# Performance work log

Hardware: AMD Instinct MI355X
Metric: run time of the kernel (lower is better)

The kernel has to match this reference:

```python
import jax, jax.numpy as jnp
import numpy as np

RANK = 16
ALPHA = 32.0
LORA_SCALE = ALPHA / RANK  # 2.0


def setup_inputs() -> dict:
    key = jax.random.key(0)
    ks = jax.random.split(key, 7)
    B_, S, D_IN, D_OUT = 4, 2048, 4096, 4096
    x = jax.random.normal(ks[0], (B_, S, D_IN), dtype=jnp.float32)
    qweight = jax.random.randint(ks[1], (D_OUT, D_IN), 0, 16, dtype=jnp.int32)
    w_min = jax.random.normal(ks[2], (D_OUT, 1), dtype=jnp.float32) * 0.1
    # row scale ~ (max-min)/15 of typical weights; keep positive
    w_scale = jax.random.uniform(ks[3], (D_OUT, 1), dtype=jnp.float32, minval=1e-3, maxval=0.02)
    bias = jax.random.normal(ks[4], (D_OUT,), dtype=jnp.float32) * 0.02
    A = jax.random.normal(ks[5], (RANK, D_IN), dtype=jnp.float32) * 0.02
    # module inits B to zeros; use small randn so the LoRA branch is exercised
    Bm = jax.random.normal(ks[6], (D_OUT, RANK), dtype=jnp.float32) * 0.02
    return {"x": x, "qweight": qweight, "w_min": w_min, "w_scale": w_scale,
            "bias": bias, "A": A, "B": Bm}


def reference(x, qweight, w_min, w_scale, bias, A, B):
    # Row-wise 4-bit dequant: W[o,i] = q[o,i]*scale[o] + min[o]
    base_weight = qweight.astype(jnp.float32) * w_scale + w_min  # [O, I]
    base_out = jnp.einsum('bsi,oi->bso', x, base_weight) + bias   # [B, S, O]
    # LoRA: (x @ A^T) @ B^T * (alpha/rank); dropout p=0 is identity
    lora_out = jnp.einsum('bsr,or->bso', jnp.einsum('bsi,ri->bsr', x, A), B) * LORA_SCALE
    return base_out + lora_out
```

## Files before the change

### kernel.cpp

```cpp
#include <hip/hip_runtime.h>
#include <hip/hip_bf16.h>

typedef unsigned short u16;
typedef unsigned int u32;
typedef __bf16 bf16x8 __attribute__((ext_vector_type(8)));
typedef float f32x4 __attribute__((ext_vector_type(4)));
typedef int i32x4 __attribute__((ext_vector_type(4)));
typedef u16 u16x4 __attribute__((ext_vector_type(4)));
typedef u16 u16x8 __attribute__((ext_vector_type(8)));

#define D_IN 4096
#define D_OUT 4096
#define M_TOT 8192
#define RANK_ 16

#define BM 256
#define BN 256
#define BK 64
#define NT (D_IN / BK)
#define OPB 2
#define DQ_BLOCKS (D_OUT / OPB)
#define XC_BLOCKS ((M_TOT * D_IN) / (256 * 8))

__device__ __forceinline__ u16 f2bf(float f) {
    union { float f; u32 u; } v; v.f = f;
    u32 u = v.u;
    u32 r = (u + 0x7FFFu + ((u >> 16) & 1u)) >> 16;
    return (u16)r;
}

__global__ __launch_bounds__(256) void producer_kernel(
        const int* __restrict__ q, const float* __restrict__ wmin,
        const float* __restrict__ wscale, const float* __restrict__ A,
        const float* __restrict__ Bm, const float* __restrict__ x,
        u16* __restrict__ Wb, u16* __restrict__ Xb) {
    const int K = D_IN;
    if (blockIdx.x < DQ_BLOCKS) {
        int o0 = blockIdx.x * OPB;
        float s0 = wscale[o0], s1 = wscale[o0 + 1];
        float m0 = wmin[o0],   m1 = wmin[o0 + 1];
        float Br0[RANK_], Br1[RANK_];
        #pragma unroll
        for (int r = 0; r < RANK_; ++r) {
            Br0[r] = 2.0f * Bm[(size_t)o0 * RANK_ + r];
            Br1[r] = 2.0f * Bm[(size_t)(o0 + 1) * RANK_ + r];
        }
        for (int i4 = threadIdx.x; i4 < K / 4; i4 += 256) {
            int i = i4 * 4;
            i32x4 q0 = __builtin_nontemporal_load((const i32x4*)(q + (size_t)o0 * K + i));
            i32x4 q1 = __builtin_nontemporal_load((const i32x4*)(q + (size_t)(o0 + 1) * K + i));
            float v00 = (float)q0.x * s0 + m0, v01 = (float)q0.y * s0 + m0;
            float v02 = (float)q0.z * s0 + m0, v03 = (float)q0.w * s0 + m0;
            float v10 = (float)q1.x * s1 + m1, v11 = (float)q1.y * s1 + m1;
            float v12 = (float)q1.z * s1 + m1, v13 = (float)q1.w * s1 + m1;
            #pragma unroll
            for (int r = 0; r < RANK_; ++r) {
                f32x4 av = *(const f32x4*)(A + (size_t)r * K + i);
                v00 += Br0[r] * av.x; v01 += Br0[r] * av.y;
                v02 += Br0[r] * av.z; v03 += Br0[r] * av.w;
                v10 += Br1[r] * av.x; v11 += Br1[r] * av.y;
                v12 += Br1[r] * av.z; v13 += Br1[r] * av.w;
            }
            u16x4 o0v, o1v;
            o0v.x = f2bf(v00); o0v.y = f2bf(v01); o0v.z = f2bf(v02); o0v.w = f2bf(v03);
            o1v.x = f2bf(v10); o1v.y = f2bf(v11); o1v.z = f2bf(v12); o1v.w = f2bf(v13);
            *(u16x4*)(Wb + (size_t)o0 * K + i) = o0v;
            *(u16x4*)(Wb + (size_t)(o0 + 1) * K + i) = o1v;
        }
    } else {
        size_t i = (size_t)(blockIdx.x - DQ_BLOCKS) * 256 + threadIdx.x;
        const f32x4* p = (const f32x4*)x + i * 2;
        f32x4 a = __builtin_nontemporal_load(p);
        f32x4 b = __builtin_nontemporal_load(p + 1);
        u16x8 o;
        o[0] = f2bf(a.x); o[1] = f2bf(a.y); o[2] = f2bf(a.z); o[3] = f2bf(a.w);
        o[4] = f2bf(b.x); o[5] = f2bf(b.y); o[6] = f2bf(b.z); o[7] = f2bf(b.w);
        *(u16x8*)(Xb + i * 8) = o;
    }
}


#define STAGE_R(sarr, larr, base, kt) do { _Pragma("unroll") \
    for (int j_ = 0; j_ < 2; ++j_) \
        __builtin_amdgcn_global_load_lds( \
            (__attribute__((address_space(1))) u32*)(sarr[j_] + (kt) * 64), \
            (__attribute__((address_space(3))) u32*)(smem + (base) + larr[j_]), \
            16, 0, 0); } while (0)

#define MFMA(d, va, vb) d = __builtin_amdgcn_mfma_f32_16x16x32_bf16(va, vb, d, 0, 0, 0)

__global__ __launch_bounds__(512, 2) void gemm_bt_kernel(const u16* __restrict__ Xb,
                                                         const u16* __restrict__ Wb,
                                                         const float* __restrict__ bias,
                                                         float* __restrict__ out) {
    extern __shared__ __align__(16) char smem[];
    const int K = D_IN, N = D_OUT;

    int bid = blockIdx.x;
    int swz = (bid & 7) * 64 + (bid >> 3);
    int tM = swz >> 4;
    int tN = swz & 15;

    int t = threadIdx.x;
    int lane = t & 63;
    int wave = t >> 6;
    int wm = wave >> 2;
    int wn = wave & 3;
    int lr = lane & 15;
    int hi = lane >> 4;
    int l7 = lane & 7;

    int xs0 = ((0 * 4 + hi) ^ l7) << 4;
    int xs1 = ((1 * 4 + hi) ^ l7) << 4;
    int aRow = (wm * 128 + lr) * 128;
    int bRow = (wn * 64 + lr) * 128;

    const u16 *srcA03[2], *srcA47[2], *srcB01[2], *srcB23[2];
    int ldsA03[2], ldsA47[2], ldsB01[2], ldsB23[2];
    #pragma unroll
    for (int j = 0; j < 2; ++j) {
        int idx = j * 512 + t;
        int rl = idx >> 3, slot = idx & 7;
        int rA = (rl & 63) + ((rl >> 6) << 7);
        int rB = (rl & 31) + ((rl >> 5) << 6);
        int r = rA;
        ldsA03[j] = r * 128 + slot * 16;
        srcA03[j] = Xb + (size_t)(tM * 256 + r) * K + ((slot ^ (r & 7)) << 3);
        r = rA + 64;
        ldsA47[j] = r * 128 + slot * 16;
        srcA47[j] = Xb + (size_t)(tM * 256 + r) * K + ((slot ^ (r & 7)) << 3);
        r = rB;
        ldsB01[j] = r * 128 + slot * 16;
        srcB01[j] = Wb + (size_t)(tN * 256 + r) * K + ((slot ^ (r & 7)) << 3);
        r = rB + 32;
        ldsB23[j] = r * 128 + slot * 16;
        srcB23[j] = Wb + (size_t)(tN * 256 + r) * K + ((slot ^ (r & 7)) << 3);
    }

    f32x4 acc[8][4];
    #pragma unroll
    for (int i = 0; i < 8; ++i)
        #pragma unroll
        for (int j = 0; j < 4; ++j)
            acc[i][j] = (f32x4){0.f, 0.f, 0.f, 0.f};

    STAGE_R(srcA03, ldsA03, 0, 0);     STAGE_R(srcA47, ldsA47, 0, 0);
    STAGE_R(srcB01, ldsB01, 65536, 0); STAGE_R(srcB23, ldsB23, 65536, 0);
    STAGE_R(srcA03, ldsA03, 32768, 1); STAGE_R(srcA47, ldsA47, 32768, 1);
    STAGE_R(srcB01, ldsB01, 98304, 1); STAGE_R(srcB23, ldsB23, 98304, 1);
    asm volatile("s_waitcnt vmcnt(8)" ::: "memory");
    __builtin_amdgcn_s_barrier();

    bf16x8 a[4][2], b23[2][2], b01[2][2];
    #pragma unroll
    for (int nf = 0; nf < 2; ++nf) {
        b01[nf][0] = *(const bf16x8*)(smem + 65536 + bRow + nf * 2048 + xs0);
        b01[nf][1] = *(const bf16x8*)(smem + 65536 + bRow + nf * 2048 + xs1);
    }
    #pragma unroll
    for (int mf = 0; mf < 4; ++mf) {
        a[mf][0] = *(const bf16x8*)(smem + aRow + mf * 2048 + xs0);
        a[mf][1] = *(const bf16x8*)(smem + aRow + mf * 2048 + xs1);
    }
    #pragma unroll
    for (int nf = 0; nf < 2; ++nf) {
        b23[nf][0] = *(const bf16x8*)(smem + 65536 + bRow + (nf + 2) * 2048 + xs0);
        b23[nf][1] = *(const bf16x8*)(smem + 65536 + bRow + (nf + 2) * 2048 + xs1);
    }

    for (int tt = 0; tt < NT; ++tt) {
        int pA = (tt & 1) * 32768;
        int pB = 65536 + (tt & 1) * 32768;
        int pBn = 65536 + ((~tt) & 1) * 32768;
        int pAn = ((~tt) & 1) * 32768;
        bool pre = (tt + 2 < NT);

        if (pre) { STAGE_R(srcB01, ldsB01, pB, tt + 2); }
        __builtin_amdgcn_s_barrier();
        asm volatile("s_waitcnt lgkmcnt(4)");
        __builtin_amdgcn_s_setprio(1);
        #pragma unroll
        for (int mf = 0; mf < 4; ++mf)
            #pragma unroll
            for (int nf = 0; nf < 2; ++nf) {
                MFMA(acc[mf][nf], a[mf][0], b01[nf][0]);
                MFMA(acc[mf][nf], a[mf][1], b01[nf][1]);
            }
        __builtin_amdgcn_s_setprio(0);
        __builtin_amdgcn_s_barrier();

        if (pre) { STAGE_R(srcA03, ldsA03, pA, tt + 2); }
        __builtin_amdgcn_s_barrier();
        asm volatile("s_waitcnt lgkmcnt(0)");
        __builtin_amdgcn_s_setprio(1);
        #pragma unroll
        for (int mf = 0; mf < 4; ++mf)
            #pragma unroll
            for (int nf = 0; nf < 2; ++nf) {
                MFMA(acc[mf][nf + 2], a[mf][0], b23[nf][0]);
                MFMA(acc[mf][nf + 2], a[mf][1], b23[nf][1]);
            }
        __builtin_amdgcn_s_setprio(0);
        #pragma unroll
        for (int mf = 0; mf < 4; ++mf) {
            a[mf][0] = *(const bf16x8*)(smem + pA + aRow + (mf + 4) * 2048 + xs0);
            a[mf][1] = *(const bf16x8*)(smem + pA + aRow + (mf + 4) * 2048 + xs1);
        }
        __builtin_amdgcn_s_barrier();

        if (pre) { STAGE_R(srcB23, ldsB23, pB, tt + 2); }
        __builtin_amdgcn_s_barrier();
        asm volatile("s_waitcnt lgkmcnt(0)");
        __builtin_amdgcn_s_setprio(1);
        #pragma unroll
        for (int mf = 0; mf < 4; ++mf)
            #pragma unroll
            for (int nf = 0; nf < 2; ++nf) {
                MFMA(acc[mf + 4][nf], a[mf][0], b01[nf][0]);
                MFMA(acc[mf + 4][nf], a[mf][1], b01[nf][1]);
            }
        __builtin_amdgcn_s_setprio(0);
        __builtin_amdgcn_s_barrier();

        if (pre) { STAGE_R(srcA47, ldsA47, pA, tt + 2); }
        if (tt < NT - 2) { asm volatile("s_waitcnt vmcnt(8)" ::: "memory"); }
        else             { asm volatile("s_waitcnt vmcnt(0)" ::: "memory"); }
        __builtin_amdgcn_s_barrier();
        if (tt + 1 < NT) {
            #pragma unroll
            for (int nf = 0; nf < 2; ++nf) {
                b01[nf][0] = *(const bf16x8*)(smem + pBn + bRow + nf * 2048 + xs0);
                b01[nf][1] = *(const bf16x8*)(smem + pBn + bRow + nf * 2048 + xs1);
            }
        }
        __builtin_amdgcn_s_setprio(1);
        #pragma unroll
        for (int mf = 0; mf < 4; ++mf)
            #pragma unroll
            for (int nf = 0; nf < 2; ++nf) {
                MFMA(acc[mf + 4][nf + 2], a[mf][0], b23[nf][0]);
                MFMA(acc[mf + 4][nf + 2], a[mf][1], b23[nf][1]);
            }
        __builtin_amdgcn_s_setprio(0);
        if (tt + 1 < NT) {
            #pragma unroll
            for (int mf = 0; mf < 4; ++mf) {
                a[mf][0] = *(const bf16x8*)(smem + pAn + aRow + mf * 2048 + xs0);
                a[mf][1] = *(const bf16x8*)(smem + pAn + aRow + mf * 2048 + xs1);
            }
            #pragma unroll
            for (int nf = 0; nf < 2; ++nf) {
                b23[nf][0] = *(const bf16x8*)(smem + pBn + bRow + (nf + 2) * 2048 + xs0);
                b23[nf][1] = *(const bf16x8*)(smem + pBn + bRow + (nf + 2) * 2048 + xs1);
            }
        }
        __builtin_amdgcn_s_barrier();
    }

    #pragma unroll
    for (int nf = 0; nf < 4; ++nf) {
        int gn = tN * 256 + wn * 64 + nf * 16 + lr;
        float bs = bias[gn];
        #pragma unroll
        for (int mf = 0; mf < 8; ++mf) {
            #pragma unroll
            for (int r = 0; r < 4; ++r) {
                int gm = tM * 256 + wm * 128 + mf * 16 + hi * 4 + r;
                out[(size_t)gm * N + gn] = acc[mf][nf][r] + bs;
            }
        }
    }
}

extern "C" void kernel_launch(void* const* d_in, const int* in_sizes, int n_in,
                              void* d_out, int out_size, void* d_ws, size_t ws_size,
                              hipStream_t stream) {
    (void)in_sizes; (void)n_in; (void)out_size; (void)ws_size;
    const float* x      = (const float*)d_in[0];
    const int*   qw     = (const int*)d_in[1];
    const float* wmin   = (const float*)d_in[2];
    const float* wscale = (const float*)d_in[3];
    const float* bias   = (const float*)d_in[4];
    const float* A      = (const float*)d_in[5];
    const float* Bm     = (const float*)d_in[6];
    float* out = (float*)d_out;

    u16* Wb = (u16*)d_ws;
    u16* Xb = Wb + (size_t)D_OUT * D_IN;

    producer_kernel<<<DQ_BLOCKS + XC_BLOCKS, 256, 0, stream>>>(
        qw, wmin, wscale, A, Bm, x, Wb, Xb);
    gemm_bt_kernel<<<(M_TOT / BM) * (D_OUT / BN), 512, 131072, stream>>>(Xb, Wb, bias, out);
}
```

Measured before the change: 276.9 us.

## Make GEMM blocks compute two N tiles each and overlap the epilogue with prefetch

The grid is halved to 256 blocks, and each block computes two output tiles in sequence: column tiles tN0 and tN0+8 for the same M row. The first K-tiles of the second tile are prefetched into LDS while the first tile's epilogue stores are written. This aims to hide the store epilogue and the pipeline warm-up behind loads and to match the grid to the CU count (256 blocks at 2 blocks per CU). The risk is a longer serial chain per block and less load balancing across CUs.

```diff
diff --git a/kernel.cpp b/kernel.cpp
--- a/kernel.cpp
+++ b/kernel.cpp
@@ -21,6 +21,7 @@
 #define OPB 2
 #define DQ_BLOCKS (D_OUT / OPB)
 #define XC_BLOCKS ((M_TOT * D_IN) / (256 * 8))
+#define PANEL ((size_t)8 * 256 * D_IN)
 
 __device__ __forceinline__ u16 f2bf(float f) {
     union { float f; u32 u; } v; v.f = f;
@@ -89,6 +90,38 @@
 
 #define MFMA(d, va, vb) d = __builtin_amdgcn_mfma_f32_16x16x32_bf16(va, vb, d, 0, 0, 0)
 
+#define PRE_READS do { \
+    _Pragma("unroll") \
+    for (int nf = 0; nf < 2; ++nf) { \
+        b01[nf][0] = *(const bf16x8*)(smem + 65536 + bRow + nf * 2048 + xs0); \
+        b01[nf][1] = *(const bf16x8*)(smem + 65536 + bRow + nf * 2048 + xs1); \
+    } \
+    _Pragma("unroll") \
+    for (int mf = 0; mf < 4; ++mf) { \
+        a[mf][0] = *(const bf16x8*)(smem + aRow + mf * 2048 + xs0); \
+        a[mf][1] = *(const bf16x8*)(smem + aRow + mf * 2048 + xs1); \
+    } \
+    _Pragma("unroll") \
+    for (int nf = 0; nf < 2; ++nf) { \
+        b23[nf][0] = *(const bf16x8*)(smem + 65536 + bRow + (nf + 2) * 2048 + xs0); \
+        b23[nf][1] = *(const bf16x8*)(smem + 65536 + bRow + (nf + 2) * 2048 + xs1); \
+    } } while (0)
+
+#define EPILOGUE(tNv) do { \
+    _Pragma("unroll") \
+    for (int nf = 0; nf < 4; ++nf) { \
+        int gn = (tNv) * 256 + wn * 64 + nf * 16 + lr; \
+        float bs = bias[gn]; \
+        _Pragma("unroll") \
+        for (int mf = 0; mf < 8; ++mf) { \
+            _Pragma("unroll") \
+            for (int r = 0; r < 4; ++r) { \
+                int gm = tM * 256 + wm * 128 + mf * 16 + hi * 4 + r; \
+                out[(size_t)gm * N + gn] = acc[mf][nf][r] + bs; \
+            } \
+        } \
+    } } while (0)
+
 __global__ __launch_bounds__(512, 2) void gemm_bt_kernel(const u16* __restrict__ Xb,
                                                          const u16* __restrict__ Wb,
                                                          const float* __restrict__ bias,
@@ -97,9 +130,9 @@
     const int K = D_IN, N = D_OUT;
 
     int bid = blockIdx.x;
-    int swz = (bid & 7) * 64 + (bid >> 3);
-    int tM = swz >> 4;
-    int tN = swz & 15;
+    int swz = (bid & 7) * 32 + (bid >> 3);
+    int tM = swz >> 3;
+    int tN0 = swz & 7;
 
     int t = threadIdx.x;
     int lane = t & 63;
@@ -131,10 +164,10 @@
         srcA47[j] = Xb + (size_t)(tM * 256 + r) * K + ((slot ^ (r & 7)) << 3);
         r = rB;
         ldsB01[j] = r * 128 + slot * 16;
-        srcB01[j] = Wb + (size_t)(tN * 256 + r) * K + ((slot ^ (r & 7)) << 3);
+        srcB01[j] = Wb + (size_t)(tN0 * 256 + r) * K + ((slot ^ (r & 7)) << 3);
         r = rB + 32;
         ldsB23[j] = r * 128 + slot * 16;
-        srcB23[j] = Wb + (size_t)(tN * 256 + r) * K + ((slot ^ (r & 7)) << 3);
+        srcB23[j] = Wb + (size_t)(tN0 * 256 + r) * K + ((slot ^ (r & 7)) << 3);
     }
 
     f32x4 acc[8][4];
@@ -152,124 +185,119 @@
     __builtin_amdgcn_s_barrier();
 
     bf16x8 a[4][2], b23[2][2], b01[2][2];
-    #pragma unroll
-    for (int nf = 0; nf < 2; ++nf) {
-        b01[nf][0] = *(const bf16x8*)(smem + 65536 + bRow + nf * 2048 + xs0);
-        b01[nf][1] = *(const bf16x8*)(smem + 65536 + bRow + nf * 2048 + xs1);
-    }
-    #pragma unroll
-    for (int mf = 0; mf < 4; ++mf) {
-        a[mf][0] = *(const bf16x8*)(smem + aRow + mf * 2048 + xs0);
-        a[mf][1] = *(const bf16x8*)(smem + aRow + mf * 2048 + xs1);
-    }
-    #pragma unroll
-    for (int nf = 0; nf < 2; ++nf) {
-        b23[nf][0] = *(const bf16x8*)(smem + 65536 + bRow + (nf + 2) * 2048 + xs0);
-        b23[nf][1] = *(const bf16x8*)(smem + 65536 + bRow + (nf + 2) * 2048 + xs1);
-    }
-
-    for (int tt = 0; tt < NT; ++tt) {
-        int pA = (tt & 1) * 32768;
-        int pB = 65536 + (tt & 1) * 32768;
-        int pBn = 65536 + ((~tt) & 1) * 32768;
-        int pAn = ((~tt) & 1) * 32768;
-        bool pre = (tt + 2 < NT);
-
-        if (pre) { STAGE_R(srcB01, ldsB01, pB, tt + 2); }
-        __builtin_amdgcn_s_barrier();
-        asm volatile("s_waitcnt lgkmcnt(4)");
-        __builtin_amdgcn_s_setprio(1);
-        #pragma unroll
-        for (int mf = 0; mf < 4; ++mf)
-            #pragma unroll
-            for (int nf = 0; nf < 2; ++nf) {
-                MFMA(acc[mf][nf], a[mf][0], b01[nf][0]);
-                MFMA(acc[mf][nf], a[mf][1], b01[nf][1]);
+    PRE_READS;
+
+    for (int rr = 0; rr < 2; ++rr) {
+        for (int tt = 0; tt < NT; ++tt) {
+            int pA = (tt & 1) * 32768;
+            int pB = 65536 + (tt & 1) * 32768;
+            int pBn = 65536 + ((~tt) & 1) * 32768;
+            int pAn = ((~tt) & 1) * 32768;
+            bool pre = (tt + 2 < NT);
+
+            if (pre) { STAGE_R(srcB01, ldsB01, pB, tt + 2); }
+            __builtin_amdgcn_s_barrier();
+            asm volatile("s_waitcnt lgkmcnt(4)");
+            __builtin_amdgcn_s_setprio(1);
+            #pragma unroll
+            for (int mf = 0; mf < 4; ++mf)
+                #pragma unroll
+                for (int nf = 0; nf < 2; ++nf) {
+                    MFMA(acc[mf][nf], a[mf][0], b01[nf][0]);
+                    MFMA(acc[mf][nf], a[mf][1], b01[nf][1]);
+                }
+            __builtin_amdgcn_s_setprio(0);
+            __builtin_amdgcn_s_barrier();
+
+            if (pre) { STAGE_R(srcA03, ldsA03, pA, tt + 2); }
+            __builtin_amdgcn_s_barrier();
+            asm volatile("s_waitcnt lgkmcnt(0)");
+            __builtin_amdgcn_s_setprio(1);
+            #pragma unroll
+            for (int mf = 0; mf < 4; ++mf)
+                #pragma unroll
+                for (int nf = 0; nf < 2; ++nf) {
+                    MFMA(acc[mf][nf + 2], a[mf][0], b23[nf][0]);
+                    MFMA(acc[mf][nf + 2], a[mf][1], b23[nf][1]);
+                }
+            __builtin_amdgcn_s_setprio(0);
+            #pragma unroll
+            for (int mf = 0; mf < 4; ++mf) {
+                a[mf][0] = *(const bf16x8*)(smem + pA + aRow + (mf + 4) * 2048 + xs0);
+                a[mf][1] = *(const bf16x8*)(smem + pA + aRow + (mf + 4) * 2048 + xs1);
             }
-        __builtin_amdgcn_s_setprio(0);
-        __builtin_amdgcn_s_barrier();
-
-        if (pre) { STAGE_R(srcA03, ldsA03, pA, tt + 2); }
-        __builtin_amdgcn_s_barrier();
-        asm volatile("s_waitcnt lgkmcnt(0)");
-        __builtin_amdgcn_s_setprio(1);
-        #pragma unroll
-        for (int mf = 0; mf < 4; ++mf)
-            #pragma unroll
-            for (int nf = 0; nf < 2; ++nf) {
-                MFMA(acc[mf][nf + 2], a[mf][0], b23[nf][0]);
-                MFMA(acc[mf][nf + 2], a[mf][1], b23[nf][1]);
+            __builtin_amdgcn_s_barrier();
+
+            if (pre) { STAGE_R(srcB23, ldsB23, pB, tt + 2); }
+            __builtin_amdgcn_s_barrier();
+            asm volatile("s_waitcnt lgkmcnt(0)");
+            __builtin_amdgcn_s_setprio(1);
+            #pragma unroll
+            for (int mf = 0; mf < 4; ++mf)
+                #pragma unroll
+                for (int nf = 0; nf < 2; ++nf) {
+                    MFMA(acc[mf + 4][nf], a[mf][0], b01[nf][0]);
+                    MFMA(acc[mf + 4][nf], a[mf][1], b01[nf][1]);
+                }
+            __builtin_amdgcn_s_setprio(0);
+            __builtin_amdgcn_s_barrier();
+
+            if (pre) { STAGE_R(srcA47, ldsA47, pA, tt + 2); }
+            if (tt < NT - 2) { asm volatile("s_waitcnt vmcnt(8)" ::: "memory"); }
+            else             { asm volatile("s_waitcnt vmcnt(0)" ::: "memory"); }
+            __builtin_amdgcn_s_barrier();
+            if (tt + 1 < NT) {
+                #pragma unroll
+                for (int nf = 0; nf < 2; ++nf) {
+                    b01[nf][0] = *(const bf16x8*)(smem + pBn + bRow + nf * 2048 + xs0);
+                    b01[nf][1] = *(const bf16x8*)(smem + pBn + bRow + nf * 2048 + xs1);
+                }
             }
-        __builtin_amdgcn_s_setprio(0);
-        #pragma unroll
-        for (int mf = 0; mf < 4; ++mf) {
-            a[mf][0] = *(const bf16x8*)(smem + pA + aRow + (mf + 4) * 2048 + xs0);
-            a[mf][1] = *(const bf16x8*)(smem + pA + aRow + (mf + 4) * 2048 + xs1);
+            __builtin_amdgcn_s_setprio(1);
+            #pragma unroll
+            for (int mf = 0; mf < 4; ++mf)
+                #pragma unroll
+                for (int nf = 0; nf < 2; ++nf) {
+                    MFMA(acc[mf + 4][nf + 2], a[mf][0], b23[nf][0]);
+                    MFMA(acc[mf + 4][nf + 2], a[mf][1], b23[nf][1]);
+                }
+            __builtin_amdgcn_s_setprio(0);
+            if (tt + 1 < NT) {
+                #pragma unroll
+                for (int mf = 0; mf < 4; ++mf) {
+                    a[mf][0] = *(const bf16x8*)(smem + pAn + aRow + mf * 2048 + xs0);
+                    a[mf][1] = *(const bf16x8*)(smem + pAn + aRow + mf * 2048 + xs1);
+                }
+                #pragma unroll
+                for (int nf = 0; nf < 2; ++nf) {
+                    b23[nf][0] = *(const bf16x8*)(smem + pBn + bRow + (nf + 2) * 2048 + xs0);
+                    b23[nf][1] = *(const bf16x8*)(smem + pBn + bRow + (nf + 2) * 2048 + xs1);
+                }
+            }
+            __builtin_amdgcn_s_barrier();
         }
-        __builtin_amdgcn_s_barrier();
-
-        if (pre) { STAGE_R(srcB23, ldsB23, pB, tt + 2); }
-        __builtin_amdgcn_s_barrier();
-        asm volatile("s_waitcnt lgkmcnt(0)");
-        __builtin_amdgcn_s_setprio(1);
-        #pragma unroll
-        for (int mf = 0; mf < 4; ++mf)
-            #pragma unroll
-            for (int nf = 0; nf < 2; ++nf) {
-                MFMA(acc[mf + 4][nf], a[mf][0], b01[nf][0]);
-                MFMA(acc[mf + 4][nf], a[mf][1], b01[nf][1]);
-            }
-        __builtin_amdgcn_s_setprio(0);
-        __builtin_amdgcn_s_barrier();
-
-        if (pre) { STAGE_R(srcA47, ldsA47, pA, tt + 2); }
-        if (tt < NT - 2) { asm volatile("s_waitcnt vmcnt(8)" ::: "memory"); }
-        else             { asm volatile("s_waitcnt vmcnt(0)" ::: "memory"); }
-        __builtin_amdgcn_s_barrier();
-        if (tt + 1 < NT) {
-            #pragma unroll
-            for (int nf = 0; nf < 2; ++nf) {
-                b01[nf][0] = *(const bf16x8*)(smem + pBn + bRow + nf * 2048 + xs0);
-                b01[nf][1] = *(const bf16x8*)(smem + pBn + bRow + nf * 2048 + xs1);
-            }
-        }
-        __builtin_amdgcn_s_setprio(1);
-        #pragma unroll
-        for (int mf = 0; mf < 4; ++mf)
-            #pragma unroll
-            for (int nf = 0; nf < 2; ++nf) {
-                MFMA(acc[mf + 4][nf + 2], a[mf][0], b23[nf][0]);
-                MFMA(acc[mf + 4][nf + 2], a[mf][1], b23[nf][1]);
-            }
-        __builtin_amdgcn_s_setprio(0);
-        if (tt + 1 < NT) {
-            #pragma unroll
-            for (int mf = 0; mf < 4; ++mf) {
-                a[mf][0] = *(const bf16x8*)(smem + pAn + aRow + mf * 2048 + xs0);
-                a[mf][1] = *(const bf16x8*)(smem + pAn + aRow + mf * 2048 + xs1);
-            }
-            #pragma unroll
-            for (int nf = 0; nf < 2; ++nf) {
-                b23[nf][0] = *(const bf16x8*)(smem + pBn + bRow + (nf + 2) * 2048 + xs0);
-                b23[nf][1] = *(const bf16x8*)(smem + pBn + bRow + (nf + 2) * 2048 + xs1);
-            }
-        }
-        __builtin_amdgcn_s_barrier();
-    }
-
-    #pragma unroll
-    for (int nf = 0; nf < 4; ++nf) {
-        int gn = tN * 256 + wn * 64 + nf * 16 + lr;
-        float bs = bias[gn];
-        #pragma unroll
-        for (int mf = 0; mf < 8; ++mf) {
-            #pragma unroll
-            for (int r = 0; r < 4; ++r) {
-                int gm = tM * 256 + wm * 128 + mf * 16 + hi * 4 + r;
-                out[(size_t)gm * N + gn] = acc[mf][nf][r] + bs;
-            }
+
+        if (rr == 0) {
+            srcB01[0] += PANEL; srcB01[1] += PANEL;
+            srcB23[0] += PANEL; srcB23[1] += PANEL;
+            STAGE_R(srcA03, ldsA03, 0, 0);     STAGE_R(srcA47, ldsA47, 0, 0);
+            STAGE_R(srcB01, ldsB01, 65536, 0); STAGE_R(srcB23, ldsB23, 65536, 0);
+            STAGE_R(srcA03, ldsA03, 32768, 1); STAGE_R(srcA47, ldsA47, 32768, 1);
+            STAGE_R(srcB01, ldsB01, 98304, 1); STAGE_R(srcB23, ldsB23, 98304, 1);
+            asm volatile("" ::: "memory");
+            EPILOGUE(tN0);
+            #pragma unroll
+            for (int i = 0; i < 8; ++i)
+                #pragma unroll
+                for (int j = 0; j < 4; ++j)
+                    acc[i][j] = (f32x4){0.f, 0.f, 0.f, 0.f};
+            asm volatile("s_waitcnt vmcnt(0)" ::: "memory");
+            __builtin_amdgcn_s_barrier();
+            PRE_READS;
         }
     }
+
+    EPILOGUE(tN0 + 8);
 }
 
 extern "C" void kernel_launch(void* const* d_in, const int* in_sizes, int n_in,
@@ -290,5 +318,5 @@
 
     producer_kernel<<<DQ_BLOCKS + XC_BLOCKS, 256, 0, stream>>>(
         qw, wmin, wscale, A, Bm, x, Wb, Xb);
-    gemm_bt_kernel<<<(M_TOT / BM) * (D_OUT / BN), 512, 131072, stream>>>(Xb, Wb, bias, out);
+    gemm_bt_kernel<<<256, 512, 131072, stream>>>(Xb, Wb, bias, out);
 }
```

New measurement: 332.0 us. +19.9%, slower.
